# Kernel optimization log

Hardware: AMD Instinct MI355X
Metric: run time of the kernel (lower is better)

Reference implementation:

```python
import jax, jax.numpy as jnp
import numpy as np

DIM = 768
HEADS = 12
HEAD_DIM = DIM // HEADS
SCALE = DIM ** (-0.5)  # NOTE: module scales by full dim, not head_dim


def setup_inputs() -> dict:
    key = jax.random.key(0)
    k1, k2, k3 = jax.random.split(key, 3)
    B, N = 4, 2048
    x = jax.random.normal(k1, (B, N, DIM), dtype=jnp.float32)
    W_qkv = jax.random.normal(k2, (DIM, 3 * DIM), dtype=jnp.float32) * (DIM ** -0.5)
    W_proj = jax.random.normal(k3, (DIM, DIM), dtype=jnp.float32) * (DIM ** -0.5)
    b_proj = jnp.zeros((DIM,), dtype=jnp.float32)
    return {"x": x, "W_qkv": W_qkv, "W_proj": W_proj, "b_proj": b_proj}


def reference(x, W_qkv, W_proj, b_proj):
    B, N, C = x.shape
    qkv = x @ W_qkv  # [B, N, 3C]
    qkv = qkv.reshape(B, N, 3, HEADS, HEAD_DIM)
    qkv = jnp.transpose(qkv, (2, 0, 3, 1, 4))  # [3, B, H, N, hd]
    q, k, v = qkv[0], qkv[1], qkv[2]
    att = jnp.einsum('bhnd,bhmd->bhnm', q, k) * SCALE
    att = jax.nn.softmax(att, axis=-1)
    # drop=0.0 -> dropout is identity
    out = jnp.einsum('bhnm,bhmd->bhnd', att, v)  # [B, H, N, hd]
    out = jnp.transpose(out, (0, 2, 1, 3)).reshape(B, N, C)
    return out @ W_proj + b_proj
```

## Files before the change

### kernel.cpp

```cpp
#include <hip/hip_runtime.h>
#include <hip/hip_bf16.h>

#define HEADS 12
#define HD    64
#define SEQ   2048
#define CDIM  768
#define QKV_SCALE 0.03608439182435161f
#define LOG2E 1.4426950408889634f
#define SM_C (QKV_SCALE * LOG2E)

typedef __attribute__((ext_vector_type(8))) short bf16x8;
typedef __attribute__((ext_vector_type(4))) float f32x4;
typedef __attribute__((ext_vector_type(4))) unsigned short usx4;
typedef __attribute__((ext_vector_type(8))) unsigned short usx8;
typedef __attribute__((ext_vector_type(2))) unsigned int uix2;
typedef __attribute__((ext_vector_type(4))) unsigned int uix4;

__device__ __forceinline__ unsigned short f2bf(float f) {
  union { __hip_bfloat16 h; unsigned short u; } c;
  c.h = __float2bfloat16(f);
  return c.u;
}

__device__ __forceinline__ float exp2_fast(float x) {
  float r; asm("v_exp_f32 %0, %1" : "=v"(r) : "v"(x)); return r;
}

__device__ __forceinline__ unsigned int cvt_pk_bf16(float lo, float hi) {
  unsigned int r; asm("v_cvt_pk_bf16_f32 %0, %1, %2" : "=v"(r) : "v"(lo), "v"(hi)); return r;
}

__device__ __forceinline__ void gload_lds16(const unsigned short* g, unsigned short* l) {
  __builtin_amdgcn_global_load_lds(
      (__attribute__((address_space(1))) void*)(g),
      (__attribute__((address_space(3))) void*)(l), 16, 0, 0);
}

__global__ __launch_bounds__(256) void k_prep(
    const float* __restrict__ x, unsigned short* __restrict__ xb,
    const float* __restrict__ Wqkv, unsigned short* __restrict__ WqkvT,
    const float* __restrict__ Wproj, unsigned short* __restrict__ WprojT) {
  __shared__ float tile[32][33];
  const int b = blockIdx.x;
  if (b < 3072) {
    int i = b * 256 + threadIdx.x;
    const float4* s4 = (const float4*)x;
    float4 a = s4[i * 2 + 0];
    float4 d = s4[i * 2 + 1];
    usx8 r;
    r[0] = f2bf(a.x); r[1] = f2bf(a.y); r[2] = f2bf(a.z); r[3] = f2bf(a.w);
    r[4] = f2bf(d.x); r[5] = f2bf(d.y); r[6] = f2bf(d.z); r[7] = f2bf(d.w);
    *(usx8*)&xb[i * 8] = r;
    return;
  }
  const float* src; unsigned short* dst; int C, c0, k0;
  if (b < 4800) {
    int tb = b - 3072;
    src = Wqkv; dst = WqkvT; C = 2304;
    c0 = (tb % 72) * 32; k0 = (tb / 72) * 32;
  } else {
    int tb = b - 4800;
    src = Wproj; dst = WprojT; C = 768;
    c0 = (tb % 24) * 32; k0 = (tb / 24) * 32;
  }
  int tx = threadIdx.x & 31;
  int ty = threadIdx.x >> 5;
#pragma unroll
  for (int i = 0; i < 32; i += 8)
    tile[ty + i][tx] = src[(size_t)(k0 + ty + i) * C + c0 + tx];
  __syncthreads();
#pragma unroll
  for (int i = 0; i < 32; i += 8)
    dst[(size_t)(c0 + ty + i) * 768 + k0 + tx] = f2bf(tile[tx][ty + i]);
}

__global__ __launch_bounds__(256, 4) void k_qkv_gemm(
    const unsigned short* __restrict__ A,
    const unsigned short* __restrict__ Bt,
    unsigned short* __restrict__ Qb, unsigned short* __restrict__ Kb,
    unsigned short* __restrict__ Vt) {
  __shared__ unsigned short As[4][128 * 32];
  __shared__ unsigned short Bs[4][128 * 32];
  const int lane = threadIdx.x & 63, w = threadIdx.x >> 6;
  const int g = lane >> 4, c = lane & 15;
  const int wm = w >> 1, wn = w & 1;
  const int id = blockIdx.y * 18 + blockIdx.x;
  const int lin = (id & 7) * 144 + (id >> 3);
  const int r0 = (lin / 18) * 128, c0 = (lin % 18) * 128;
  f32x4 acc[4][4] = {};

  const unsigned short* aptr[2];
  const unsigned short* bptr[2];
#pragma unroll
  for (int i = 0; i < 2; ++i) {
    int e = (w * 2 + i) * 512 + lane * 8;
    int row = e >> 5;
    int cc = ((e >> 3) & 3) ^ ((row >> 1) & 3);
    aptr[i] = A  + (size_t)(r0 + row) * 768 + cc * 8;
    bptr[i] = Bt + (size_t)(c0 + row) * 768 + cc * 8;
  }

  const int sg = g ^ ((c >> 1) & 3);
  int offA[4], offB[4];
#pragma unroll
  for (int f = 0; f < 4; ++f) {
    offA[f] = (wm * 64 + f * 16 + c) * 32 + sg * 8;
    offB[f] = (wn * 64 + f * 16 + c) * 32 + sg * 8;
  }

  auto STAGE = [&](int k0, int b) {
#pragma unroll
    for (int i = 0; i < 2; ++i) {
      gload_lds16(aptr[i] + k0, &As[b][(w * 2 + i) * 512]);
      gload_lds16(bptr[i] + k0, &Bs[b][(w * 2 + i) * 512]);
    }
  };

  STAGE(0, 0);
  STAGE(32, 1);
  asm volatile("s_waitcnt vmcnt(4)" ::: "memory");
  __builtin_amdgcn_s_barrier();

#pragma unroll
  for (int t = 0; t < 24; ++t) {
    if (t + 2 < 24) {
      STAGE((t + 2) * 32, (t + 2) & 3);
      asm volatile("s_waitcnt vmcnt(8)" ::: "memory");
    } else if (t + 2 == 24) {
      asm volatile("s_waitcnt vmcnt(4)" ::: "memory");
    } else {
      asm volatile("s_waitcnt vmcnt(0)" ::: "memory");
    }
    __builtin_amdgcn_s_barrier();

    const int buf = t & 3;
    bf16x8 af[4], bfr[4];
#pragma unroll
    for (int f = 0; f < 4; ++f) {
      af[f]  = *(const bf16x8*)&As[buf][offA[f]];
      bfr[f] = *(const bf16x8*)&Bs[buf][offB[f]];
    }
    __builtin_amdgcn_s_setprio(1);
#pragma unroll
    for (int fm = 0; fm < 4; ++fm)
#pragma unroll
      for (int fn = 0; fn < 4; ++fn)
        acc[fm][fn] = __builtin_amdgcn_mfma_f32_16x16x32_bf16(af[fm], bfr[fn], acc[fm][fn], 0, 0, 0);
    __builtin_amdgcn_s_setprio(0);
  }

  const int which = c0 / 768;
  const float qsc = (which == 0) ? SM_C : 1.0f;
#pragma unroll
  for (int fm = 0; fm < 4; ++fm) {
    int gr0 = r0 + wm * 64 + fm * 16 + ((lane >> 4) << 2);
    int bb = gr0 >> 11, n0 = gr0 & 2047;
#pragma unroll
    for (int fn = 0; fn < 4; ++fn) {
      int gc = c0 + wn * 64 + fn * 16 + (lane & 15);
      int rem = gc - which * 768;
      int h = rem >> 6, d = rem & 63;
      int bh = bb * HEADS + h;
      f32x4 v = acc[fm][fn];
      if (which == 2) {
        usx4 p;
        p[0] = f2bf(v[0]); p[1] = f2bf(v[1]); p[2] = f2bf(v[2]); p[3] = f2bf(v[3]);
        *(usx4*)&Vt[(size_t)(bh * 64 + d) * 2048 + n0] = p;
      } else {
        unsigned short* dst = (which == 0 ? Qb : Kb) + (size_t)(bh * 2048 + n0) * 64 + d;
        dst[0]   = f2bf(v[0] * qsc);
        dst[64]  = f2bf(v[1] * qsc);
        dst[128] = f2bf(v[2] * qsc);
        dst[192] = f2bf(v[3] * qsc);
      }
    }
  }
}

__global__ __launch_bounds__(256, 2) void k_attn(
    const unsigned short* __restrict__ Qb, const unsigned short* __restrict__ Kb,
    const unsigned short* __restrict__ Vt, unsigned short* __restrict__ Ob) {
  __shared__ unsigned short Ksm[2][64 * 64];
  __shared__ unsigned short Vsm[2][64 * 64];
  const int lane = threadIdx.x & 63, w = threadIdx.x >> 6;
  const int g = lane >> 4, c = lane & 15;

  int id = blockIdx.x + (blockIdx.y << 4);
  int lin = (id & 7) * 96 + (id >> 3);
  int bx = lin & 15, bh = lin >> 4;
  const int q0 = bx * 128 + w * 32;
  const int bb = bh / HEADS, h = bh % HEADS;

  const unsigned short* Qp = Qb + (size_t)bh * SEQ * HD;
  const unsigned short* Kp = Kb + (size_t)bh * SEQ * HD;
  const unsigned short* Vp = Vt + (size_t)bh * HD * SEQ;

  bf16x8 aQ[2][2];
#pragma unroll
  for (int qf = 0; qf < 2; ++qf)
#pragma unroll
    for (int ks = 0; ks < 2; ++ks)
      aQ[qf][ks] = *(const bf16x8*)&Qp[(size_t)(q0 + qf * 16 + c) * 64 + ks * 32 + g * 8];

  float lrun[2] = {0.f, 0.f};
  f32x4 accOT[4][2] = {};
  const f32x4 fzero = {0.f, 0.f, 0.f, 0.f};

  int offf[2][4];
#pragma unroll
  for (int ks = 0; ks < 2; ++ks)
#pragma unroll
    for (int f = 0; f < 4; ++f) {
      int row = f * 16 + c;
      offf[ks][f] = row * 64 + (((ks * 4 + g) ^ (row & 7)) * 8);
    }

  const int eo0 = (w * 2 + 0) * 512 + lane * 8;
  const int row0 = eo0 >> 6, cc0 = ((eo0 >> 3) & 7) ^ (row0 & 7);
  const int eo1 = (w * 2 + 1) * 512 + lane * 8;
  const int row1 = eo1 >> 6, cc1 = ((eo1 >> 3) & 7) ^ (row1 & 7);
  const unsigned short* kga = Kp + (size_t)row0 * 64 + cc0 * 8;
  const unsigned short* kgb = Kp + (size_t)row1 * 64 + cc1 * 8;
  const unsigned short* vga = Vp + (size_t)row0 * 2048 + cc0 * 8;
  const unsigned short* vgb = Vp + (size_t)row1 * 2048 + cc1 * 8;

  gload_lds16(kga, &Ksm[0][(w * 2 + 0) * 512]);
  gload_lds16(kgb, &Ksm[0][(w * 2 + 1) * 512]);
  gload_lds16(vga, &Vsm[0][(w * 2 + 0) * 512]);
  gload_lds16(vgb, &Vsm[0][(w * 2 + 1) * 512]);
  asm volatile("s_waitcnt vmcnt(0)" ::: "memory");
  __syncthreads();

  auto TILE = [&](int t, int buf) {
    if (t + 1 < 32) {
      gload_lds16(kga + (t + 1) * 4096, &Ksm[buf ^ 1][(w * 2 + 0) * 512]);
      gload_lds16(kgb + (t + 1) * 4096, &Ksm[buf ^ 1][(w * 2 + 1) * 512]);
      gload_lds16(vga + (t + 1) * 64,   &Vsm[buf ^ 1][(w * 2 + 0) * 512]);
      gload_lds16(vgb + (t + 1) * 64,   &Vsm[buf ^ 1][(w * 2 + 1) * 512]);
    }

    bf16x8 kf0[4], kf1[4];
#pragma unroll
    for (int fm = 0; fm < 4; ++fm) {
      kf0[fm] = *(const bf16x8*)&Ksm[buf][offf[0][fm]];
      kf1[fm] = *(const bf16x8*)&Ksm[buf][offf[1][fm]];
    }
    f32x4 st[4][2];
    __builtin_amdgcn_s_setprio(1);
#pragma unroll
    for (int fm = 0; fm < 4; ++fm)
#pragma unroll
      for (int qf = 0; qf < 2; ++qf)
        st[fm][qf] = __builtin_amdgcn_mfma_f32_16x16x32_bf16(kf0[fm], aQ[qf][0], fzero, 0, 0, 0);
#pragma unroll
    for (int fm = 0; fm < 4; ++fm)
#pragma unroll
      for (int qf = 0; qf < 2; ++qf)
        st[fm][qf] = __builtin_amdgcn_mfma_f32_16x16x32_bf16(kf1[fm], aQ[qf][1], st[fm][qf], 0, 0, 0);
    __builtin_amdgcn_s_setprio(0);

    uix4 pfrag[2][2];
#pragma unroll
    for (int qf = 0; qf < 2; ++qf) {
      float p[4][4];
      float ts[4];
#pragma unroll
      for (int fm = 0; fm < 4; ++fm) {
        p[fm][0] = exp2_fast(st[fm][qf][0]);
        p[fm][1] = exp2_fast(st[fm][qf][1]);
        p[fm][2] = exp2_fast(st[fm][qf][2]);
        p[fm][3] = exp2_fast(st[fm][qf][3]);
        ts[fm] = (p[fm][0] + p[fm][1]) + (p[fm][2] + p[fm][3]);
      }
      lrun[qf] += (ts[0] + ts[1]) + (ts[2] + ts[3]);

#pragma unroll
      for (int ks = 0; ks < 2; ++ks)
#pragma unroll
        for (int tt = 0; tt < 2; ++tt) {
          unsigned int a = cvt_pk_bf16(p[2 * ks][2 * tt], p[2 * ks][2 * tt + 1]);
          unsigned int b = cvt_pk_bf16(p[2 * ks + 1][2 * tt], p[2 * ks + 1][2 * tt + 1]);
          uix2 s1 = __builtin_amdgcn_permlane32_swap(a, b, false, false);
          uix2 s2 = __builtin_amdgcn_permlane16_swap(s1[0], s1[1], false, false);
          pfrag[ks][qf][tt] = s2[0];
          pfrag[ks][qf][2 + tt] = s2[1];
        }
    }

    bf16x8 vf0[4], vf1[4];
#pragma unroll
    for (int fd = 0; fd < 4; ++fd) {
      vf0[fd] = *(const bf16x8*)&Vsm[buf][offf[0][fd]];
      vf1[fd] = *(const bf16x8*)&Vsm[buf][offf[1][fd]];
    }
    __builtin_amdgcn_s_setprio(1);
#pragma unroll
    for (int fd = 0; fd < 4; ++fd)
#pragma unroll
      for (int qf = 0; qf < 2; ++qf) {
        accOT[fd][qf] = __builtin_amdgcn_mfma_f32_16x16x32_bf16(
            vf0[fd], *(const bf16x8*)&pfrag[0][qf], accOT[fd][qf], 0, 0, 0);
        accOT[fd][qf] = __builtin_amdgcn_mfma_f32_16x16x32_bf16(
            vf1[fd], *(const bf16x8*)&pfrag[1][qf], accOT[fd][qf], 0, 0, 0);
      }
    __builtin_amdgcn_s_setprio(0);

    asm volatile("s_waitcnt vmcnt(0)" ::: "memory");
    __syncthreads();
  };

  for (int kt = 0; kt < 32; kt += 2) {
    TILE(kt, 0);
    TILE(kt + 1, 1);
  }

#pragma unroll
  for (int qf = 0; qf < 2; ++qf) {
    float l = lrun[qf];
    l += __shfl_xor(l, 16);
    l += __shfl_xor(l, 32);
    float rl = 1.0f / l;
    int n = q0 + qf * 16 + c;
#pragma unroll
    for (int fd = 0; fd < 4; ++fd) {
      f32x4 v = accOT[fd][qf];
      usx4 pk;
      pk[0] = f2bf(v[0] * rl); pk[1] = f2bf(v[1] * rl);
      pk[2] = f2bf(v[2] * rl); pk[3] = f2bf(v[3] * rl);
      *(usx4*)&Ob[(size_t)(bb * SEQ + n) * CDIM + h * HD + fd * 16 + 4 * g] = pk;
    }
  }
}

__global__ __launch_bounds__(256, 3) void k_proj_gemm(
    const unsigned short* __restrict__ A,
    const unsigned short* __restrict__ Bt,
    const float* __restrict__ bias, float* __restrict__ out) {
  __shared__ unsigned short As[4][64 * 32];
  __shared__ unsigned short Bs[4][128 * 32];
  const int lane = threadIdx.x & 63, w = threadIdx.x >> 6;
  const int g = lane >> 4, c = lane & 15;
  const int wm = w & 1, wn = w >> 1;
  const int id = blockIdx.y * 6 + blockIdx.x;
  const int lin = (id & 7) * 96 + (id >> 3);
  const int r0 = (lin / 6) * 64, c0 = (lin % 6) * 128;
  f32x4 acc[2][4] = {};

  const unsigned short* aptr;
  {
    int e = w * 512 + lane * 8;
    int row = e >> 5;
    int cc = ((e >> 3) & 3) ^ ((row >> 1) & 3);
    aptr = A + (size_t)(r0 + row) * 768 + cc * 8;
  }
  const unsigned short* bptr[2];
#pragma unroll
  for (int i = 0; i < 2; ++i) {
    int e = (w * 2 + i) * 512 + lane * 8;
    int row = e >> 5;
    int cc = ((e >> 3) & 3) ^ ((row >> 1) & 3);
    bptr[i] = Bt + (size_t)(c0 + row) * 768 + cc * 8;
  }

  const int sg = g ^ ((c >> 1) & 3);
  int offA[2], offB[4];
#pragma unroll
  for (int f = 0; f < 2; ++f) offA[f] = (wm * 32 + f * 16 + c) * 32 + sg * 8;
#pragma unroll
  for (int f = 0; f < 4; ++f) offB[f] = (wn * 64 + f * 16 + c) * 32 + sg * 8;

  auto STAGE = [&](int k0, int b) {
    gload_lds16(aptr + k0, &As[b][w * 512]);
#pragma unroll
    for (int i = 0; i < 2; ++i)
      gload_lds16(bptr[i] + k0, &Bs[b][(w * 2 + i) * 512]);
  };

  STAGE(0, 0);
  STAGE(32, 1);
  asm volatile("s_waitcnt vmcnt(3)" ::: "memory");
  __builtin_amdgcn_s_barrier();

#pragma unroll
  for (int t = 0; t < 24; ++t) {
    if (t + 2 < 24) {
      STAGE((t + 2) * 32, (t + 2) & 3);
      asm volatile("s_waitcnt vmcnt(6)" ::: "memory");
    } else if (t + 2 == 24) {
      asm volatile("s_waitcnt vmcnt(3)" ::: "memory");
    } else {
      asm volatile("s_waitcnt vmcnt(0)" ::: "memory");
    }
    __builtin_amdgcn_s_barrier();

    const int buf = t & 3;
    bf16x8 af[2], bfr[4];
#pragma unroll
    for (int f = 0; f < 2; ++f) af[f] = *(const bf16x8*)&As[buf][offA[f]];
#pragma unroll
    for (int f = 0; f < 4; ++f) bfr[f] = *(const bf16x8*)&Bs[buf][offB[f]];
    __builtin_amdgcn_s_setprio(1);
#pragma unroll
    for (int fm = 0; fm < 2; ++fm)
#pragma unroll
      for (int fn = 0; fn < 4; ++fn)
        acc[fm][fn] = __builtin_amdgcn_mfma_f32_16x16x32_bf16(af[fm], bfr[fn], acc[fm][fn], 0, 0, 0);
    __builtin_amdgcn_s_setprio(0);
  }

#pragma unroll
  for (int fm = 0; fm < 2; ++fm) {
    int gr0 = r0 + wm * 32 + fm * 16 + ((lane >> 4) << 2);
#pragma unroll
    for (int fn = 0; fn < 4; ++fn) {
      int gc = c0 + wn * 64 + fn * 16 + (lane & 15);
      float bsv = bias[gc];
      f32x4 v = acc[fm][fn];
#pragma unroll
      for (int r = 0; r < 4; ++r)
        out[(size_t)(gr0 + r) * CDIM + gc] = v[r] + bsv;
    }
  }
}

extern "C" void kernel_launch(void* const* d_in, const int* in_sizes, int n_in,
                              void* d_out, int out_size, void* d_ws, size_t ws_size,
                              hipStream_t stream) {
  const float* x      = (const float*)d_in[0];
  const float* W_qkv  = (const float*)d_in[1];
  const float* W_proj = (const float*)d_in[2];
  const float* b_proj = (const float*)d_in[3];
  float* out = (float*)d_out;

  unsigned short* ws     = (unsigned short*)d_ws;
  unsigned short* xb     = ws;
  unsigned short* WqkvT  = xb + 6291456;
  unsigned short* WprojT = WqkvT + 1769472;
  unsigned short* Qb     = WprojT + 589824;
  unsigned short* Kb     = Qb + 6291456;
  unsigned short* Vt     = Kb + 6291456;
  unsigned short* Ob     = Vt + 6291456;

  k_prep<<<5376, 256, 0, stream>>>(x, xb, W_qkv, WqkvT, W_proj, WprojT);
  k_qkv_gemm<<<dim3(18, 64), 256, 0, stream>>>(xb, WqkvT, Qb, Kb, Vt);
  k_attn<<<dim3(16, 48), 256, 0, stream>>>(Qb, Kb, Vt, Ob);
  k_proj_gemm<<<dim3(6, 128), 256, 0, stream>>>(Ob, WprojT, b_proj, out);
}
```

Baseline: 140.0 us.

## Shrink QKV GEMM tile to 64x128 with single-buffered 64-wide K steps

The QKV projection GEMM moves from a 128x128 tile with a 4-stage async LDS pipeline over 32-wide K slices to a 64x128 tile with one LDS buffer and 64-wide K steps. The launch grid doubles to 2304 blocks, and the XOR swizzle is adapted to the new row width. The aim is more blocks and better CU occupancy and wave balance. In exchange, global-load/compute overlap is lost: every K step now waits for vmcnt(0) and syncs twice, and each A/B byte loaded feeds fewer MFMAs.

```diff
diff --git a/kernel.cpp b/kernel.cpp
--- a/kernel.cpp
+++ b/kernel.cpp
@@ -74,90 +74,79 @@
     dst[(size_t)(c0 + ty + i) * 768 + k0 + tx] = f2bf(tile[tx][ty + i]);
 }
 
-__global__ __launch_bounds__(256, 4) void k_qkv_gemm(
+__global__ __launch_bounds__(256) void k_qkv_gemm(
     const unsigned short* __restrict__ A,
     const unsigned short* __restrict__ Bt,
     unsigned short* __restrict__ Qb, unsigned short* __restrict__ Kb,
     unsigned short* __restrict__ Vt) {
-  __shared__ unsigned short As[4][128 * 32];
-  __shared__ unsigned short Bs[4][128 * 32];
+  __shared__ unsigned short As[64 * 64];
+  __shared__ unsigned short Bs[128 * 64];
   const int lane = threadIdx.x & 63, w = threadIdx.x >> 6;
   const int g = lane >> 4, c = lane & 15;
-  const int wm = w >> 1, wn = w & 1;
+  const int wm = w & 1, wn = w >> 1;
   const int id = blockIdx.y * 18 + blockIdx.x;
-  const int lin = (id & 7) * 144 + (id >> 3);
-  const int r0 = (lin / 18) * 128, c0 = (lin % 18) * 128;
-  f32x4 acc[4][4] = {};
+  const int lin = (id & 7) * 288 + (id >> 3);
+  const int r0 = (lin / 18) * 64, c0 = (lin % 18) * 128;
+  f32x4 acc[2][4] = {};
 
   const unsigned short* aptr[2];
-  const unsigned short* bptr[2];
+  const unsigned short* bptr[4];
 #pragma unroll
   for (int i = 0; i < 2; ++i) {
     int e = (w * 2 + i) * 512 + lane * 8;
-    int row = e >> 5;
-    int cc = ((e >> 3) & 3) ^ ((row >> 1) & 3);
-    aptr[i] = A  + (size_t)(r0 + row) * 768 + cc * 8;
+    int row = e >> 6, cc = ((e >> 3) & 7) ^ (row & 7);
+    aptr[i] = A + (size_t)(r0 + row) * 768 + cc * 8;
+  }
+#pragma unroll
+  for (int i = 0; i < 4; ++i) {
+    int e = (w * 4 + i) * 512 + lane * 8;
+    int row = e >> 6, cc = ((e >> 3) & 7) ^ (row & 7);
     bptr[i] = Bt + (size_t)(c0 + row) * 768 + cc * 8;
   }
 
-  const int sg = g ^ ((c >> 1) & 3);
-  int offA[4], offB[4];
-#pragma unroll
-  for (int f = 0; f < 4; ++f) {
-    offA[f] = (wm * 64 + f * 16 + c) * 32 + sg * 8;
-    offB[f] = (wn * 64 + f * 16 + c) * 32 + sg * 8;
-  }
-
-  auto STAGE = [&](int k0, int b) {
-#pragma unroll
-    for (int i = 0; i < 2; ++i) {
-      gload_lds16(aptr[i] + k0, &As[b][(w * 2 + i) * 512]);
-      gload_lds16(bptr[i] + k0, &Bs[b][(w * 2 + i) * 512]);
-    }
-  };
-
-  STAGE(0, 0);
-  STAGE(32, 1);
-  asm volatile("s_waitcnt vmcnt(4)" ::: "memory");
-  __builtin_amdgcn_s_barrier();
-
-#pragma unroll
-  for (int t = 0; t < 24; ++t) {
-    if (t + 2 < 24) {
-      STAGE((t + 2) * 32, (t + 2) & 3);
-      asm volatile("s_waitcnt vmcnt(8)" ::: "memory");
-    } else if (t + 2 == 24) {
-      asm volatile("s_waitcnt vmcnt(4)" ::: "memory");
-    } else {
-      asm volatile("s_waitcnt vmcnt(0)" ::: "memory");
-    }
-    __builtin_amdgcn_s_barrier();
-
-    const int buf = t & 3;
-    bf16x8 af[4], bfr[4];
-#pragma unroll
-    for (int f = 0; f < 4; ++f) {
-      af[f]  = *(const bf16x8*)&As[buf][offA[f]];
-      bfr[f] = *(const bf16x8*)&Bs[buf][offB[f]];
-    }
-    __builtin_amdgcn_s_setprio(1);
-#pragma unroll
-    for (int fm = 0; fm < 4; ++fm)
-#pragma unroll
-      for (int fn = 0; fn < 4; ++fn)
-        acc[fm][fn] = __builtin_amdgcn_mfma_f32_16x16x32_bf16(af[fm], bfr[fn], acc[fm][fn], 0, 0, 0);
-    __builtin_amdgcn_s_setprio(0);
+  for (int k0 = 0; k0 < 768; k0 += 64) {
+#pragma unroll
+    for (int i = 0; i < 2; ++i)
+      gload_lds16(aptr[i] + k0, &As[(w * 2 + i) * 512]);
+#pragma unroll
+    for (int i = 0; i < 4; ++i)
+      gload_lds16(bptr[i] + k0, &Bs[(w * 4 + i) * 512]);
+    asm volatile("s_waitcnt vmcnt(0)" ::: "memory");
+    __syncthreads();
+
+#pragma unroll
+    for (int ks = 0; ks < 2; ++ks) {
+      bf16x8 af[2], bfr[4];
+#pragma unroll
+      for (int f = 0; f < 2; ++f) {
+        int ar = wm * 32 + f * 16 + c;
+        int ac = (ks * 4 + g) ^ (ar & 7);
+        af[f] = *(const bf16x8*)&As[ar * 64 + ac * 8];
+      }
+#pragma unroll
+      for (int f = 0; f < 4; ++f) {
+        int br = wn * 64 + f * 16 + c;
+        int bc = (ks * 4 + g) ^ (br & 7);
+        bfr[f] = *(const bf16x8*)&Bs[br * 64 + bc * 8];
+      }
+#pragma unroll
+      for (int fm = 0; fm < 2; ++fm)
+#pragma unroll
+        for (int fn = 0; fn < 4; ++fn)
+          acc[fm][fn] = __builtin_amdgcn_mfma_f32_16x16x32_bf16(af[fm], bfr[fn], acc[fm][fn], 0, 0, 0);
+    }
+    __syncthreads();
   }
 
   const int which = c0 / 768;
   const float qsc = (which == 0) ? SM_C : 1.0f;
 #pragma unroll
-  for (int fm = 0; fm < 4; ++fm) {
-    int gr0 = r0 + wm * 64 + fm * 16 + ((lane >> 4) << 2);
+  for (int fm = 0; fm < 2; ++fm) {
+    int gr0 = r0 + wm * 32 + fm * 16 + ((lane >> 4) << 2);
     int bb = gr0 >> 11, n0 = gr0 & 2047;
 #pragma unroll
     for (int fn = 0; fn < 4; ++fn) {
-      int gc = c0 + wn * 64 + fn * 16 + (lane & 15);
+      int gc = c0 + wn * 64 + fn * 16 + c;
       int rem = gc - which * 768;
       int h = rem >> 6, d = rem & 63;
       int bh = bb * HEADS + h;
@@ -442,7 +431,7 @@
   unsigned short* Ob     = Vt + 6291456;
 
   k_prep<<<5376, 256, 0, stream>>>(x, xb, W_qkv, WqkvT, W_proj, WprojT);
-  k_qkv_gemm<<<dim3(18, 64), 256, 0, stream>>>(xb, WqkvT, Qb, Kb, Vt);
+  k_qkv_gemm<<<dim3(18, 128), 256, 0, stream>>>(xb, WqkvT, Qb, Kb, Vt);
   k_attn<<<dim3(16, 48), 256, 0, stream>>>(Qb, Kb, Vt, Ob);
   k_proj_gemm<<<dim3(6, 128), 256, 0, stream>>>(Ob, WprojT, b_proj, out);
 }
```

Result: faster. 132.2 us (-5.5%).
